# Optimization experiments

Measured on AMD Instinct MI355X. Metric: run time of the kernel, lower is better.

## Reference

```python
import jax, jax.numpy as jnp
import numpy as np

N, E, B, NUM_NODES = 80000, 1280000, 8, 10000
D_IN, H, EMB, ATT, OUT = 64, 64, 64, 64, 1


def setup_inputs() -> dict:
    key = jax.random.key(0)
    ks = jax.random.split(key, 12)
    x = jax.random.normal(ks[0], (N, D_IN), dtype=jnp.float32)
    edge_index = jax.random.randint(ks[1], (2, E), 0, N, dtype=jnp.int64)
    edge_weight = jax.random.uniform(ks[2], (E,), dtype=jnp.float32)
    batch = jnp.repeat(jnp.arange(B, dtype=jnp.int64), NUM_NODES)
    app_embedding = jax.random.normal(ks[3], (B, 1, EMB), dtype=jnp.float32)
    def lin(k, fi, fo):
        bound = 1.0 / np.sqrt(fi)
        k1, k2 = jax.random.split(k)
        W = jax.random.uniform(k1, (fi, fo), minval=-bound, maxval=bound, dtype=jnp.float32)
        b = jax.random.uniform(k2, (fo,), minval=-bound, maxval=bound, dtype=jnp.float32)
        return W, b
    W1, b1 = lin(ks[4], D_IN, H)
    W2, b2 = lin(ks[5], H, H)
    Wa, ba = lin(ks[6], H + EMB, ATT)
    Ws, bs = lin(ks[7], ATT, 1)
    Wo, bo = lin(ks[8], H, OUT)
    return dict(x=x, edge_index=edge_index, edge_weight=edge_weight, batch=batch,
                app_embedding=app_embedding, W1=W1, b1=b1, W2=W2, b2=b2,
                Wa=Wa, ba=ba, Ws=Ws, bs=bs, Wo=Wo, bo=bo)


def gcn_conv(x, row, col, ew, W, b):
    # PyG GCNConv: add self-loops (weight 1), symmetric normalization
    n = x.shape[0]
    xw = x @ W                                            # [N, H]
    deg = jax.ops.segment_sum(ew, col, num_segments=n) + 1.0  # self-loop adds 1
    dis = jax.lax.rsqrt(deg)                              # deg >= 1
    norm = dis[row] * ew * dis[col]                       # [E]
    agg = jax.ops.segment_sum(norm[:, None] * xw[row], col, num_segments=n)
    return agg + (dis * dis)[:, None] * xw + b            # self-loop term + bias


def reference(x, edge_index, edge_weight, batch, app_embedding,
              W1, b1, W2, b2, Wa, ba, Ws, bs, Wo, bo):
    row, col = edge_index[0], edge_index[1]
    h = jax.nn.relu(gcn_conv(x, row, col, edge_weight, W1, b1))
    h = jax.nn.relu(gcn_conv(h, row, col, edge_weight, W2, b2))
    emb = app_embedding[:, 0, :][batch]                   # [N, EMB]
    combined = jnp.concatenate([h, emb], axis=-1)         # [N, H+EMB]
    att_hidden = jax.nn.leaky_relu(combined @ Wa + ba, negative_slope=0.2)
    scores = att_hidden @ Ws + bs                         # [N, 1]
    weights = jax.nn.softmax(scores, axis=0)              # softmax over all nodes
    node_out = (weights * h) @ Wo + bo                    # [N, OUT=1]
    flat = node_out.reshape(-1)                           # [N] since OUT=1
    sums = jax.ops.segment_sum(flat, batch, num_segments=B)
    counts = jax.ops.segment_sum(jnp.ones_like(flat), batch, num_segments=B)
    return sums / counts                                  # global_mean_pool -> [B]
```

## Files before the change

### kernel.cpp

```cpp
#include <hip/hip_runtime.h>
#include <hip/hip_fp16.h>
#include <math.h>


#define DEG_SCALE 16777216.0f
#define DEG_INV   (1.0f / 16777216.0f)
#define M48       0xFFFFFFFFFFFFULL
#define MAXDEG    64

typedef __attribute__((ext_vector_type(8))) _Float16 h8;
typedef __attribute__((ext_vector_type(4))) float f32x4;


__global__ __launch_bounds__(256) void front_kernel(
    const float* __restrict__ x, const float* __restrict__ W1,
    __half* __restrict__ Y, int N,
    const int* __restrict__ ei, const float* __restrict__ ew,
    unsigned long long* __restrict__ packed, unsigned int* __restrict__ epack2,
    int E, int nG) {
  int bid = (int)blockIdx.x;
  bool isGemm = (bid % 5 == 0) && (bid / 5 < nG);
  if (!isGemm) {
    int gBefore = (bid + 4) / 5; if (gBefore > nG) gBefore = nG;
    int di = bid - gBefore;
    int e = di * 256 + threadIdx.x;
    if (e >= E) return;
    int row = ei[e];
    int col = ei[E + e];
    float w = ew[e];
    unsigned long long q = (unsigned long long)(w * DEG_SCALE + 0.5f);
    unsigned long long old = atomicAdd(&packed[col], (1ULL << 48) | q);
    unsigned rank = (unsigned)(old >> 48);
    unsigned q15 = (unsigned)(w * 32768.0f + 0.5f);
    if (q15 > 32767u) q15 = 32767u;
    if (rank < MAXDEG)
      epack2[(size_t)col * MAXDEG + rank] = ((unsigned)row << 15) | q15;
    return;
  }
  int gb = bid / 5;
  __shared__ float wlds[64][65];
  int t = threadIdx.x;
  for (int i = t; i < 4096; i += 256) wlds[i >> 6][i & 63] = W1[i];
  __syncthreads();
  int lane = t & 63, wave = t >> 6;
  int sub = lane & 15, grp = lane >> 4;
  int r0 = gb * 64 + wave * 16;
  h8 bf[2][4];
#pragma unroll
  for (int kk = 0; kk < 2; ++kk)
#pragma unroll
    for (int f = 0; f < 4; ++f)
#pragma unroll
      for (int i = 0; i < 8; ++i)
        bf[kk][f][i] = (_Float16)wlds[kk * 32 + grp * 8 + i][f * 16 + sub];
  int arow = r0 + sub; if (arow >= N) arow = N - 1;
  const float4* xr = (const float4*)(x + (size_t)arow * 64 + grp * 8);
  float4 u0 = xr[0], u1 = xr[1];
  const float4* xr2 = (const float4*)(x + (size_t)arow * 64 + 32 + grp * 8);
  float4 v0 = xr2[0], v1 = xr2[1];
  h8 a0, a1;
  a0[0]=(_Float16)u0.x; a0[1]=(_Float16)u0.y; a0[2]=(_Float16)u0.z; a0[3]=(_Float16)u0.w;
  a0[4]=(_Float16)u1.x; a0[5]=(_Float16)u1.y; a0[6]=(_Float16)u1.z; a0[7]=(_Float16)u1.w;
  a1[0]=(_Float16)v0.x; a1[1]=(_Float16)v0.y; a1[2]=(_Float16)v0.z; a1[3]=(_Float16)v0.w;
  a1[4]=(_Float16)v1.x; a1[5]=(_Float16)v1.y; a1[6]=(_Float16)v1.z; a1[7]=(_Float16)v1.w;
  f32x4 zero = {0.f, 0.f, 0.f, 0.f};
  f32x4 acc[4] = {zero, zero, zero, zero};
#pragma unroll
  for (int f = 0; f < 4; ++f) {
    acc[f] = __builtin_amdgcn_mfma_f32_16x16x32_f16(a0, bf[0][f], acc[f], 0, 0, 0);
    acc[f] = __builtin_amdgcn_mfma_f32_16x16x32_f16(a1, bf[1][f], acc[f], 0, 0, 0);
  }
  _Float16* Yp = (_Float16*)Y;
#pragma unroll
  for (int f = 0; f < 4; ++f)
#pragma unroll
    for (int j = 0; j < 4; ++j) {
      int orow = r0 + grp * 4 + j;
      if (orow < N) Yp[(size_t)orow * 64 + f * 16 + sub] = (_Float16)acc[f][j];
    }
}

__global__ __launch_bounds__(256) void mid_kernel(
    const unsigned long long* __restrict__ packed, __half* __restrict__ xw,
    float* __restrict__ dis, int N,
    const float* __restrict__ emb, const float* __restrict__ Wa,
    const float* __restrict__ ba, float* __restrict__ pre, int B, int gS) {
  if ((int)blockIdx.x >= gS) {
    int t = ((int)blockIdx.x - gS) * 256 + threadIdx.x;
    if (t >= B * 64) return;
    int b = t >> 6, j = t & 63;
    float s = ba[j];
    for (int k = 0; k < 64; ++k)
      s = fmaf(emb[b * 64 + k], Wa[(64 + k) * 64 + j], s);
    pre[t] = s;
    return;
  }
  int idx = blockIdx.x * 256 + threadIdx.x;
  if (idx >= N * 8) return;
  int row = idx >> 3;
  int off = idx & 7;
  unsigned long long p = packed[row];
  float d = rsqrtf((float)(long long)(p & M48) * DEG_INV + 1.0f);
  if (off == 0) dis[row] = d;
  h8* ptr = (h8*)(xw + (size_t)row * 64) + off;
  h8 v = *ptr;
  h8 o;
#pragma unroll
  for (int i = 0; i < 8; ++i) o[i] = (_Float16)((float)v[i] * d);
  *ptr = o;
}

__global__ __launch_bounds__(256) void agg_fused_kernel(
    const __half* __restrict__ xw, const unsigned int* __restrict__ epack2,
    const unsigned long long* __restrict__ packed,
    const float* __restrict__ bias, __half* __restrict__ h, int N) {
  int wid = (blockIdx.x * 256 + threadIdx.x) >> 6;
  int lane = threadIdx.x & 63;
  if (wid >= N) return;
  int q = lane >> 3, sub = lane & 7;
  unsigned long long p = packed[wid];
  int cnt = (int)(p >> 48);
  if (cnt > MAXDEG) cnt = MAXDEG;
  float dis_c = rsqrtf((float)(long long)(p & M48) * DEG_INV + 1.0f);
  int start = wid * MAXDEG;
  int end = start + cnt;
  float acc[8];
#pragma unroll
  for (int i = 0; i < 8; ++i) acc[i] = 0.f;
  int t = start + q;
  for (; t + 8 < end; t += 16) {
    unsigned w0 = epack2[t];
    unsigned w1 = epack2[t + 8];
    h8 v0 = *(const h8*)(xw + ((size_t)(w0 >> 15)) * 64 + sub * 8);
    h8 v1 = *(const h8*)(xw + ((size_t)(w1 >> 15)) * 64 + sub * 8);
    float c0 = (float)(w0 & 0x7FFFu) * (1.0f / 32768.0f);
    float c1 = (float)(w1 & 0x7FFFu) * (1.0f / 32768.0f);
#pragma unroll
    for (int i = 0; i < 8; ++i) acc[i] = fmaf(c0, (float)v0[i], acc[i]);
#pragma unroll
    for (int i = 0; i < 8; ++i) acc[i] = fmaf(c1, (float)v1[i], acc[i]);
  }
  if (t < end) {
    unsigned w0 = epack2[t];
    h8 v0 = *(const h8*)(xw + ((size_t)(w0 >> 15)) * 64 + sub * 8);
    float c0 = (float)(w0 & 0x7FFFu) * (1.0f / 32768.0f);
#pragma unroll
    for (int i = 0; i < 8; ++i) acc[i] = fmaf(c0, (float)v0[i], acc[i]);
  }
#pragma unroll
  for (int i = 0; i < 8; ++i) {
    acc[i] += __shfl_xor(acc[i], 8, 64);
    acc[i] += __shfl_xor(acc[i], 16, 64);
    acc[i] += __shfl_xor(acc[i], 32, 64);
  }
  if (q == 0) {
    h8 self = *(const h8*)(xw + (size_t)wid * 64 + sub * 8);
    h8 o;
#pragma unroll
    for (int i = 0; i < 8; ++i)
      o[i] = (_Float16)fmaxf(dis_c * (acc[i] + (float)self[i]) + bias[sub * 8 + i], 0.f);
    *(h8*)(h + (size_t)wid * 64 + sub * 8) = o;
  }
}

__global__ __launch_bounds__(256) void gemm_mfma_f16_scaled(
    const __half* __restrict__ X, const float* __restrict__ W,
    const float* __restrict__ dis, __half* __restrict__ Y, int N) {
  __shared__ float wlds[64][65];
  int t = threadIdx.x;
  for (int i = t; i < 4096; i += 256) wlds[i >> 6][i & 63] = W[i];
  __syncthreads();
  int lane = t & 63, wave = t >> 6;
  int sub = lane & 15, grp = lane >> 4;
  int r0 = (int)blockIdx.x * 64 + wave * 16;
  h8 bf[2][4];
#pragma unroll
  for (int kk = 0; kk < 2; ++kk)
#pragma unroll
    for (int f = 0; f < 4; ++f)
#pragma unroll
      for (int i = 0; i < 8; ++i)
        bf[kk][f][i] = (_Float16)wlds[kk * 32 + grp * 8 + i][f * 16 + sub];
  int arow = r0 + sub; if (arow >= N) arow = N - 1;
  const _Float16* Xp = (const _Float16*)X;
  h8 a0 = *(const h8*)(Xp + (size_t)arow * 64 + grp * 8);
  h8 a1 = *(const h8*)(Xp + (size_t)arow * 64 + 32 + grp * 8);
  f32x4 zero = {0.f, 0.f, 0.f, 0.f};
  f32x4 acc[4] = {zero, zero, zero, zero};
#pragma unroll
  for (int f = 0; f < 4; ++f) {
    acc[f] = __builtin_amdgcn_mfma_f32_16x16x32_f16(a0, bf[0][f], acc[f], 0, 0, 0);
    acc[f] = __builtin_amdgcn_mfma_f32_16x16x32_f16(a1, bf[1][f], acc[f], 0, 0, 0);
  }
  _Float16* Yp = (_Float16*)Y;
#pragma unroll
  for (int j = 0; j < 4; ++j) {
    int orow = r0 + grp * 4 + j;
    if (orow < N) {
      float d = dis[orow];
#pragma unroll
      for (int f = 0; f < 4; ++f)
        Yp[(size_t)orow * 64 + f * 16 + sub] = (_Float16)(acc[f][j] * d);
    }
  }
}

__global__ __launch_bounds__(256) void att_mfma_kernel(
    const __half* __restrict__ h2, const int* __restrict__ bat,
    const float* __restrict__ Wa, const float* __restrict__ Ws,
    const float* __restrict__ bs, const float* __restrict__ pre,
    const float* __restrict__ Wo,
    float* __restrict__ bmax, float* __restrict__ bsum,
    float* __restrict__ pd0, float* __restrict__ pd1, int N) {
  __shared__ float wlds[64][65];
  __shared__ float pr[8][64];
  __shared__ float wov[64];
  __shared__ float redm[4], reds[4], redp0[4], redp1[4];
  __shared__ int sb0sh;
  int t = threadIdx.x;
  for (int i = t; i < 4096; i += 256) wlds[i >> 6][i & 63] = Wa[i];
  for (int i = t; i < 512; i += 256) pr[i >> 6][i & 63] = pre[i];
  if (t < 64) wov[t] = Wo[t];
  if (t == 0) sb0sh = bat[blockIdx.x * 64];
  __syncthreads();
  int lane = t & 63, wave = t >> 6;
  int sub = lane & 15, grp = lane >> 4;
  int r0 = (int)blockIdx.x * 64 + wave * 16;
  h8 bf[2][4];
#pragma unroll
  for (int kk = 0; kk < 2; ++kk)
#pragma unroll
    for (int f = 0; f < 4; ++f)
#pragma unroll
      for (int i = 0; i < 8; ++i)
        bf[kk][f][i] = (_Float16)wlds[kk * 32 + grp * 8 + i][f * 16 + sub];
  float wsf[4];
#pragma unroll
  for (int f = 0; f < 4; ++f) wsf[f] = Ws[f * 16 + sub];
  float bs0 = bs[0];
  int arow = r0 + sub; if (arow >= N) arow = N - 1;
  const _Float16* Xp = (const _Float16*)h2;
  h8 a0 = *(const h8*)(Xp + (size_t)arow * 64 + grp * 8);
  h8 a1 = *(const h8*)(Xp + (size_t)arow * 64 + 32 + grp * 8);
  float dp = 0.f;
#pragma unroll
  for (int i = 0; i < 8; ++i) {
    dp = fmaf((float)a0[i], wov[grp * 8 + i], dp);
    dp = fmaf((float)a1[i], wov[32 + grp * 8 + i], dp);
  }
  dp += __shfl_xor(dp, 16, 64);
  dp += __shfl_xor(dp, 32, 64);
  f32x4 zero = {0.f, 0.f, 0.f, 0.f};
  f32x4 acc[4] = {zero, zero, zero, zero};
#pragma unroll
  for (int f = 0; f < 4; ++f) {
    acc[f] = __builtin_amdgcn_mfma_f32_16x16x32_f16(a0, bf[0][f], acc[f], 0, 0, 0);
    acc[f] = __builtin_amdgcn_mfma_f32_16x16x32_f16(a1, bf[1][f], acc[f], 0, 0, 0);
  }
  int sb0 = sb0sh;
  float sloc[4];
  int bl[4];
  float mloc = -3.4e38f;
#pragma unroll
  for (int j = 0; j < 4; ++j) {
    int row = r0 + grp * 4 + j;
    int rc = (row < N) ? row : N - 1;
    int b = bat[rc];
    bl[j] = b;
    float s = 0.f;
#pragma unroll
    for (int f = 0; f < 4; ++f) {
      float v = acc[f][j] + pr[b][f * 16 + sub];
      v = (v > 0.f) ? v : 0.2f * v;
      s = fmaf(v, wsf[f], s);
    }
    s += __shfl_xor(s, 1, 64); s += __shfl_xor(s, 2, 64);
    s += __shfl_xor(s, 4, 64); s += __shfl_xor(s, 8, 64);
    s += bs0;
    sloc[j] = (row < N) ? s : -3.4e38f;
    mloc = fmaxf(mloc, sloc[j]);
  }
  for (int off = 32; off; off >>= 1) mloc = fmaxf(mloc, __shfl_xor(mloc, off, 64));
  if (lane == 0) redm[wave] = mloc;
  __syncthreads();
  float bm = fmaxf(fmaxf(redm[0], redm[1]), fmaxf(redm[2], redm[3]));
  float dj[4];
#pragma unroll
  for (int j = 0; j < 4; ++j) dj[j] = __shfl(dp, grp * 4 + j, 64);
  float es = 0.f, p0 = 0.f, p1 = 0.f;
  if (sub == 0) {
#pragma unroll
    for (int j = 0; j < 4; ++j) {
      if (sloc[j] > -3.0e38f) {
        float e = expf(sloc[j] - bm);
        es += e;
        float v = e * dj[j];
        if (bl[j] == sb0) p0 += v; else p1 += v;
      }
    }
  }
  for (int off = 32; off; off >>= 1) {
    es += __shfl_xor(es, off, 64);
    p0 += __shfl_xor(p0, off, 64);
    p1 += __shfl_xor(p1, off, 64);
  }
  if (lane == 0) { reds[wave] = es; redp0[wave] = p0; redp1[wave] = p1; }
  __syncthreads();
  if (t == 0) {
    bmax[blockIdx.x] = bm;
    bsum[blockIdx.x] = reds[0] + reds[1] + reds[2] + reds[3];
    pd0[blockIdx.x] = redp0[0] + redp0[1] + redp0[2] + redp0[3];
    pd1[blockIdx.x] = redp1[0] + redp1[1] + redp1[2] + redp1[3];
  }
}

__global__ __launch_bounds__(256) void tail_kernel(
    const float* __restrict__ bmax, const float* __restrict__ bsum,
    const float* __restrict__ pd0, const float* __restrict__ pd1,
    int nb, int npb, const float* __restrict__ bo, float* __restrict__ out, int B) {
  __shared__ float lds[4];
  __shared__ float Msh, Zsh;
  __shared__ float accs[9];
  int t = threadIdx.x;
  if (t < 9) accs[t] = 0.f;
  float m = -3.4e38f;
  for (int k = t; k < nb; k += 256) m = fmaxf(m, bmax[k]);
  for (int off = 32; off; off >>= 1) m = fmaxf(m, __shfl_xor(m, off, 64));
  if ((t & 63) == 0) lds[t >> 6] = m;
  __syncthreads();
  if (t == 0) Msh = fmaxf(fmaxf(lds[0], lds[1]), fmaxf(lds[2], lds[3]));
  __syncthreads();
  float M = Msh;
  float z = 0.f;
  for (int k = t; k < nb; k += 256) {
    float e = expf(bmax[k] - M);
    z += bsum[k] * e;
    int b0 = (k * 64) / npb;
    float v0 = pd0[k] * e;
    float v1 = pd1[k] * e;
    if (v0 != 0.f) atomicAdd(&accs[b0], v0);
    if (v1 != 0.f) atomicAdd(&accs[b0 + 1], v1);
  }
  for (int off = 32; off; off >>= 1) z += __shfl_xor(z, off, 64);
  if ((t & 63) == 0) lds[t >> 6] = z;
  __syncthreads();
  if (t == 0) Zsh = lds[0] + lds[1] + lds[2] + lds[3];
  __syncthreads();
  if (t < B) out[t] = accs[t] / Zsh / (float)npb + bo[0];
}

extern "C" void kernel_launch(void* const* d_in, const int* in_sizes, int n_in,
                              void* d_out, int out_size, void* d_ws, size_t ws_size,
                              hipStream_t stream) {
  const float* x   = (const float*)d_in[0];
  const int*   ei  = (const int*)d_in[1];
  const float* ew  = (const float*)d_in[2];
  const int*   bat = (const int*)d_in[3];
  const float* emb = (const float*)d_in[4];
  const float* W1  = (const float*)d_in[5];
  const float* b1  = (const float*)d_in[6];
  const float* W2  = (const float*)d_in[7];
  const float* b2  = (const float*)d_in[8];
  const float* Wa  = (const float*)d_in[9];
  const float* ba  = (const float*)d_in[10];
  const float* Ws  = (const float*)d_in[11];
  const float* bs  = (const float*)d_in[12];
  const float* Wo  = (const float*)d_in[13];
  const float* bo  = (const float*)d_in[14];
  float* out = (float*)d_out;

  const int N = in_sizes[0] / 64;
  const int E = in_sizes[2];
  const int B = in_sizes[4] / 64;

  float* ws = (float*)d_ws;
  size_t o = 0;
  unsigned long long* packed = (unsigned long long*)(ws + o); o += 2 * (size_t)N;
  unsigned int* epack2 = (unsigned int*)(ws + o); o += (size_t)N * MAXDEG;
  __half* bufA   = (__half*)(ws + o); o += (size_t)N * 32;
  __half* bufB   = (__half*)(ws + o); o += (size_t)N * 32;
  float* dis     = ws + o; o += N;
  float* pre     = ws + o; o += 512;
  float* bmaxa   = ws + o; o += 2048;
  float* bsuma   = ws + o; o += 2048;
  float* pd0a    = ws + o; o += 2048;
  float* pd1a    = ws + o; o += 2048;

  hipMemsetAsync(packed, 0, (size_t)(2 * N) * sizeof(float), stream);

  int gE = (E + 255) / 256;
  int gW = (N * 64 + 255) / 256;
  int gM = (N + 63) / 64;
  int gS = (N * 8 + 255) / 256;
  int gP = (B * 64 + 255) / 256;

  front_kernel<<<gM + gE, 256, 0, stream>>>(x, W1, bufA, N, ei, ew, packed, epack2, E, gM);

  mid_kernel<<<gS + gP, 256, 0, stream>>>(packed, bufA, dis, N, emb, Wa, ba, pre, B, gS);

  agg_fused_kernel<<<gW, 256, 0, stream>>>(bufA, epack2, packed, b1, bufB, N);
  gemm_mfma_f16_scaled<<<gM, 256, 0, stream>>>(bufB, W2, dis, bufA, N);
  agg_fused_kernel<<<gW, 256, 0, stream>>>(bufA, epack2, packed, b2, bufB, N);

  att_mfma_kernel<<<gM, 256, 0, stream>>>(bufB, bat, Wa, Ws, bs, pre, Wo,
                                          bmaxa, bsuma, pd0a, pd1a, N);
  tail_kernel<<<1, 256, 0, stream>>>(bmaxa, bsuma, pd0a, pd1a, gM, N / B, bo, out, B);
}
```

Baseline: 199.4 us.

## Fuse GCN aggregation with following dense layers and drop pre-scaling pass

After: 371.6 us. 86.4% more time.

```diff
diff --git a/kernel.cpp b/kernel.cpp
--- a/kernel.cpp
+++ b/kernel.cpp
@@ -7,10 +7,10 @@
 #define DEG_INV   (1.0f / 16777216.0f)
 #define M48       0xFFFFFFFFFFFFULL
 #define MAXDEG    64
+#define NPB       32
 
 typedef __attribute__((ext_vector_type(8))) _Float16 h8;
 typedef __attribute__((ext_vector_type(4))) float f32x4;
-
 
 __global__ __launch_bounds__(256) void front_kernel(
     const float* __restrict__ x, const float* __restrict__ W1,
@@ -80,13 +80,12 @@
     }
 }
 
-__global__ __launch_bounds__(256) void mid_kernel(
-    const unsigned long long* __restrict__ packed, __half* __restrict__ xw,
-    float* __restrict__ dis, int N,
+__global__ __launch_bounds__(256) void mid2_kernel(
+    const unsigned long long* __restrict__ packed, float* __restrict__ dis, int N,
     const float* __restrict__ emb, const float* __restrict__ Wa,
-    const float* __restrict__ ba, float* __restrict__ pre, int B, int gS) {
-  if ((int)blockIdx.x >= gS) {
-    int t = ((int)blockIdx.x - gS) * 256 + threadIdx.x;
+    const float* __restrict__ ba, float* __restrict__ pre, int B, int gD) {
+  if ((int)blockIdx.x >= gD) {
+    int t = ((int)blockIdx.x - gD) * 256 + threadIdx.x;
     if (t >= B * 64) return;
     int b = t >> 6, j = t & 63;
     float s = ba[j];
@@ -95,55 +94,41 @@
     pre[t] = s;
     return;
   }
-  int idx = blockIdx.x * 256 + threadIdx.x;
-  if (idx >= N * 8) return;
-  int row = idx >> 3;
-  int off = idx & 7;
-  unsigned long long p = packed[row];
-  float d = rsqrtf((float)(long long)(p & M48) * DEG_INV + 1.0f);
-  if (off == 0) dis[row] = d;
-  h8* ptr = (h8*)(xw + (size_t)row * 64) + off;
-  h8 v = *ptr;
-  h8 o;
-#pragma unroll
-  for (int i = 0; i < 8; ++i) o[i] = (_Float16)((float)v[i] * d);
-  *ptr = o;
-}
-
-__global__ __launch_bounds__(256) void agg_fused_kernel(
+  int i = blockIdx.x * 256 + threadIdx.x;
+  if (i >= N) return;
+  unsigned long long p = packed[i];
+  dis[i] = rsqrtf((float)(long long)(p & M48) * DEG_INV + 1.0f);
+}
+
+__device__ __forceinline__ void gather_node(
     const __half* __restrict__ xw, const unsigned int* __restrict__ epack2,
-    const unsigned long long* __restrict__ packed,
-    const float* __restrict__ bias, __half* __restrict__ h, int N) {
-  int wid = (blockIdx.x * 256 + threadIdx.x) >> 6;
-  int lane = threadIdx.x & 63;
-  if (wid >= N) return;
-  int q = lane >> 3, sub = lane & 7;
-  unsigned long long p = packed[wid];
-  int cnt = (int)(p >> 48);
-  if (cnt > MAXDEG) cnt = MAXDEG;
-  float dis_c = rsqrtf((float)(long long)(p & M48) * DEG_INV + 1.0f);
+    const float* __restrict__ dis, int wid, int cnt, int q, int sub,
+    float acc[8]) {
+#pragma unroll
+  for (int i = 0; i < 8; ++i) acc[i] = 0.f;
   int start = wid * MAXDEG;
   int end = start + cnt;
-  float acc[8];
-#pragma unroll
-  for (int i = 0; i < 8; ++i) acc[i] = 0.f;
-  int t = start + q;
-  for (; t + 8 < end; t += 16) {
-    unsigned w0 = epack2[t];
-    unsigned w1 = epack2[t + 8];
-    h8 v0 = *(const h8*)(xw + ((size_t)(w0 >> 15)) * 64 + sub * 8);
-    h8 v1 = *(const h8*)(xw + ((size_t)(w1 >> 15)) * 64 + sub * 8);
-    float c0 = (float)(w0 & 0x7FFFu) * (1.0f / 32768.0f);
-    float c1 = (float)(w1 & 0x7FFFu) * (1.0f / 32768.0f);
+  int e = start + q;
+  for (; e + 8 < end; e += 16) {
+    unsigned w0 = epack2[e];
+    unsigned w1 = epack2[e + 8];
+    int r0 = (int)(w0 >> 15), r1 = (int)(w1 >> 15);
+    float d0 = dis[r0], d1 = dis[r1];
+    h8 v0 = *(const h8*)(xw + (size_t)r0 * 64 + sub * 8);
+    h8 v1 = *(const h8*)(xw + (size_t)r1 * 64 + sub * 8);
+    float c0 = (float)(w0 & 0x7FFFu) * (1.0f / 32768.0f) * d0;
+    float c1 = (float)(w1 & 0x7FFFu) * (1.0f / 32768.0f) * d1;
 #pragma unroll
     for (int i = 0; i < 8; ++i) acc[i] = fmaf(c0, (float)v0[i], acc[i]);
 #pragma unroll
     for (int i = 0; i < 8; ++i) acc[i] = fmaf(c1, (float)v1[i], acc[i]);
   }
-  if (t < end) {
-    unsigned w0 = epack2[t];
-    h8 v0 = *(const h8*)(xw + ((size_t)(w0 >> 15)) * 64 + sub * 8);
-    float c0 = (float)(w0 & 0x7FFFu) * (1.0f / 32768.0f);
+  if (e < end) {
+    unsigned w0 = epack2[e];
+    int r0 = (int)(w0 >> 15);
+    float d0 = dis[r0];
+    h8 v0 = *(const h8*)(xw + (size_t)r0 * 64 + sub * 8);
+    float c0 = (float)(w0 & 0x7FFFu) * (1.0f / 32768.0f) * d0;
 #pragma unroll
     for (int i = 0; i < 8; ++i) acc[i] = fmaf(c0, (float)v0[i], acc[i]);
   }
@@ -153,164 +138,127 @@
     acc[i] += __shfl_xor(acc[i], 16, 64);
     acc[i] += __shfl_xor(acc[i], 32, 64);
   }
-  if (q == 0) {
+}
+
+__global__ __launch_bounds__(256) void conv_gemm_kernel(
+    const __half* __restrict__ xw, const unsigned int* __restrict__ epack2,
+    const unsigned long long* __restrict__ packed, const float* __restrict__ dis,
+    const float* __restrict__ b1, const float* __restrict__ W2,
+    __half* __restrict__ xw2, int N) {
+  __shared__ float w2[64][65];
+  int t = threadIdx.x;
+  for (int i = t; i < 4096; i += 256) w2[i >> 6][i & 63] = W2[i];
+  __syncthreads();
+  int lane = t & 63, wave = t >> 6;
+  int q = lane >> 3, sub = lane & 7;
+  float bias[8];
+#pragma unroll
+  for (int i = 0; i < 8; ++i) bias[i] = b1[sub * 8 + i];
+  int base = (int)blockIdx.x * NPB;
+  for (int n = wave; n < NPB; n += 4) {
+    int wid = base + n;
+    if (wid >= N) break;
+    unsigned long long p = packed[wid];
+    int cnt = (int)(p >> 48); if (cnt > MAXDEG) cnt = MAXDEG;
+    float dis_c = dis[wid];
+    float acc[8];
+    gather_node(xw, epack2, dis, wid, cnt, q, sub, acc);
     h8 self = *(const h8*)(xw + (size_t)wid * 64 + sub * 8);
-    h8 o;
+    float dc2 = dis_c * dis_c;
+    float h1v[8];
 #pragma unroll
     for (int i = 0; i < 8; ++i)
-      o[i] = (_Float16)fmaxf(dis_c * (acc[i] + (float)self[i]) + bias[sub * 8 + i], 0.f);
-    *(h8*)(h + (size_t)wid * 64 + sub * 8) = o;
-  }
-}
-
-__global__ __launch_bounds__(256) void gemm_mfma_f16_scaled(
-    const __half* __restrict__ X, const float* __restrict__ W,
-    const float* __restrict__ dis, __half* __restrict__ Y, int N) {
-  __shared__ float wlds[64][65];
-  int t = threadIdx.x;
-  for (int i = t; i < 4096; i += 256) wlds[i >> 6][i & 63] = W[i];
-  __syncthreads();
-  int lane = t & 63, wave = t >> 6;
-  int sub = lane & 15, grp = lane >> 4;
-  int r0 = (int)blockIdx.x * 64 + wave * 16;
-  h8 bf[2][4];
-#pragma unroll
-  for (int kk = 0; kk < 2; ++kk)
-#pragma unroll
-    for (int f = 0; f < 4; ++f)
+      h1v[i] = fmaxf(fmaf(dis_c, acc[i], fmaf(dc2, (float)self[i], bias[i])), 0.f);
+    float y = 0.f;
+#pragma unroll
+    for (int s = 0; s < 8; ++s)
 #pragma unroll
       for (int i = 0; i < 8; ++i)
-        bf[kk][f][i] = (_Float16)wlds[kk * 32 + grp * 8 + i][f * 16 + sub];
-  int arow = r0 + sub; if (arow >= N) arow = N - 1;
-  const _Float16* Xp = (const _Float16*)X;
-  h8 a0 = *(const h8*)(Xp + (size_t)arow * 64 + grp * 8);
-  h8 a1 = *(const h8*)(Xp + (size_t)arow * 64 + 32 + grp * 8);
-  f32x4 zero = {0.f, 0.f, 0.f, 0.f};
-  f32x4 acc[4] = {zero, zero, zero, zero};
-#pragma unroll
-  for (int f = 0; f < 4; ++f) {
-    acc[f] = __builtin_amdgcn_mfma_f32_16x16x32_f16(a0, bf[0][f], acc[f], 0, 0, 0);
-    acc[f] = __builtin_amdgcn_mfma_f32_16x16x32_f16(a1, bf[1][f], acc[f], 0, 0, 0);
-  }
-  _Float16* Yp = (_Float16*)Y;
-#pragma unroll
-  for (int j = 0; j < 4; ++j) {
-    int orow = r0 + grp * 4 + j;
-    if (orow < N) {
-      float d = dis[orow];
-#pragma unroll
-      for (int f = 0; f < 4; ++f)
-        Yp[(size_t)orow * 64 + f * 16 + sub] = (_Float16)(acc[f][j] * d);
-    }
-  }
-}
-
-__global__ __launch_bounds__(256) void att_mfma_kernel(
-    const __half* __restrict__ h2, const int* __restrict__ bat,
+        y = fmaf(__shfl(h1v[i], s, 64), w2[s * 8 + i][lane], y);
+    ((_Float16*)xw2)[(size_t)wid * 64 + lane] = (_Float16)y;
+  }
+}
+
+__global__ __launch_bounds__(256) void conv_att_kernel(
+    const __half* __restrict__ xw2, const unsigned int* __restrict__ epack2,
+    const unsigned long long* __restrict__ packed, const float* __restrict__ dis,
+    const float* __restrict__ b2, const int* __restrict__ bat,
     const float* __restrict__ Wa, const float* __restrict__ Ws,
     const float* __restrict__ bs, const float* __restrict__ pre,
     const float* __restrict__ Wo,
     float* __restrict__ bmax, float* __restrict__ bsum,
     float* __restrict__ pd0, float* __restrict__ pd1, int N) {
-  __shared__ float wlds[64][65];
+  __shared__ float wa[64][65];
   __shared__ float pr[8][64];
-  __shared__ float wov[64];
-  __shared__ float redm[4], reds[4], redp0[4], redp1[4];
+  __shared__ float wsv[64], wov[64];
+  __shared__ float cm[4], cz[4], cp0[4], cp1[4];
   __shared__ int sb0sh;
   int t = threadIdx.x;
-  for (int i = t; i < 4096; i += 256) wlds[i >> 6][i & 63] = Wa[i];
+  for (int i = t; i < 4096; i += 256) wa[i >> 6][i & 63] = Wa[i];
   for (int i = t; i < 512; i += 256) pr[i >> 6][i & 63] = pre[i];
-  if (t < 64) wov[t] = Wo[t];
-  if (t == 0) sb0sh = bat[blockIdx.x * 64];
+  if (t < 64) { wsv[t] = Ws[t]; wov[t] = Wo[t]; }
+  if (t == 0) sb0sh = bat[(size_t)blockIdx.x * NPB];
   __syncthreads();
   int lane = t & 63, wave = t >> 6;
-  int sub = lane & 15, grp = lane >> 4;
-  int r0 = (int)blockIdx.x * 64 + wave * 16;
-  h8 bf[2][4];
-#pragma unroll
-  for (int kk = 0; kk < 2; ++kk)
-#pragma unroll
-    for (int f = 0; f < 4; ++f)
-#pragma unroll
-      for (int i = 0; i < 8; ++i)
-        bf[kk][f][i] = (_Float16)wlds[kk * 32 + grp * 8 + i][f * 16 + sub];
-  float wsf[4];
-#pragma unroll
-  for (int f = 0; f < 4; ++f) wsf[f] = Ws[f * 16 + sub];
+  int q = lane >> 3, sub = lane & 7;
+  float bias[8];
+#pragma unroll
+  for (int i = 0; i < 8; ++i) bias[i] = b2[sub * 8 + i];
   float bs0 = bs[0];
-  int arow = r0 + sub; if (arow >= N) arow = N - 1;
-  const _Float16* Xp = (const _Float16*)h2;
-  h8 a0 = *(const h8*)(Xp + (size_t)arow * 64 + grp * 8);
-  h8 a1 = *(const h8*)(Xp + (size_t)arow * 64 + 32 + grp * 8);
-  float dp = 0.f;
-#pragma unroll
-  for (int i = 0; i < 8; ++i) {
-    dp = fmaf((float)a0[i], wov[grp * 8 + i], dp);
-    dp = fmaf((float)a1[i], wov[32 + grp * 8 + i], dp);
-  }
-  dp += __shfl_xor(dp, 16, 64);
-  dp += __shfl_xor(dp, 32, 64);
-  f32x4 zero = {0.f, 0.f, 0.f, 0.f};
-  f32x4 acc[4] = {zero, zero, zero, zero};
-#pragma unroll
-  for (int f = 0; f < 4; ++f) {
-    acc[f] = __builtin_amdgcn_mfma_f32_16x16x32_f16(a0, bf[0][f], acc[f], 0, 0, 0);
-    acc[f] = __builtin_amdgcn_mfma_f32_16x16x32_f16(a1, bf[1][f], acc[f], 0, 0, 0);
-  }
   int sb0 = sb0sh;
-  float sloc[4];
-  int bl[4];
-  float mloc = -3.4e38f;
-#pragma unroll
-  for (int j = 0; j < 4; ++j) {
-    int row = r0 + grp * 4 + j;
-    int rc = (row < N) ? row : N - 1;
-    int b = bat[rc];
-    bl[j] = b;
-    float s = 0.f;
-#pragma unroll
-    for (int f = 0; f < 4; ++f) {
-      float v = acc[f][j] + pr[b][f * 16 + sub];
-      v = (v > 0.f) ? v : 0.2f * v;
-      s = fmaf(v, wsf[f], s);
+  float m = -3.4e38f, z = 0.f, p0 = 0.f, p1 = 0.f;
+  int base = (int)blockIdx.x * NPB;
+  for (int n = wave; n < NPB; n += 4) {
+    int wid = base + n;
+    if (wid >= N) break;
+    unsigned long long p = packed[wid];
+    int cnt = (int)(p >> 48); if (cnt > MAXDEG) cnt = MAXDEG;
+    float dis_c = dis[wid];
+    float acc[8];
+    gather_node(xw2, epack2, dis, wid, cnt, q, sub, acc);
+    h8 self = *(const h8*)(xw2 + (size_t)wid * 64 + sub * 8);
+    float dc2 = dis_c * dis_c;
+    float h2v[8];
+#pragma unroll
+    for (int i = 0; i < 8; ++i)
+      h2v[i] = fmaxf(fmaf(dis_c, acc[i], fmaf(dc2, (float)self[i], bias[i])), 0.f);
+    int b = bat[wid];
+    float y = pr[b][lane];
+    float dp = 0.f;
+#pragma unroll
+    for (int s = 0; s < 8; ++s)
+#pragma unroll
+      for (int i = 0; i < 8; ++i) {
+        float hv = __shfl(h2v[i], s, 64);
+        y = fmaf(hv, wa[s * 8 + i][lane], y);
+        dp = fmaf(hv, wov[s * 8 + i], dp);
+      }
+    float a = ((y > 0.f) ? y : 0.2f * y) * wsv[lane];
+    a += __shfl_xor(a, 1, 64);  a += __shfl_xor(a, 2, 64);
+    a += __shfl_xor(a, 4, 64);  a += __shfl_xor(a, 8, 64);
+    a += __shfl_xor(a, 16, 64); a += __shfl_xor(a, 32, 64);
+    float s_r = a + bs0;
+    if (s_r > m) {
+      float r = expf(m - s_r);
+      z *= r; p0 *= r; p1 *= r; m = s_r;
     }
-    s += __shfl_xor(s, 1, 64); s += __shfl_xor(s, 2, 64);
-    s += __shfl_xor(s, 4, 64); s += __shfl_xor(s, 8, 64);
-    s += bs0;
-    sloc[j] = (row < N) ? s : -3.4e38f;
-    mloc = fmaxf(mloc, sloc[j]);
-  }
-  for (int off = 32; off; off >>= 1) mloc = fmaxf(mloc, __shfl_xor(mloc, off, 64));
-  if (lane == 0) redm[wave] = mloc;
-  __syncthreads();
-  float bm = fmaxf(fmaxf(redm[0], redm[1]), fmaxf(redm[2], redm[3]));
-  float dj[4];
-#pragma unroll
-  for (int j = 0; j < 4; ++j) dj[j] = __shfl(dp, grp * 4 + j, 64);
-  float es = 0.f, p0 = 0.f, p1 = 0.f;
-  if (sub == 0) {
-#pragma unroll
-    for (int j = 0; j < 4; ++j) {
-      if (sloc[j] > -3.0e38f) {
-        float e = expf(sloc[j] - bm);
-        es += e;
-        float v = e * dj[j];
-        if (bl[j] == sb0) p0 += v; else p1 += v;
-      }
+    float e = expf(s_r - m);
+    z += e;
+    float v = e * dp;
+    if (b == sb0) p0 += v; else p1 += v;
+  }
+  if (lane == 0) { cm[wave] = m; cz[wave] = z; cp0[wave] = p0; cp1[wave] = p1; }
+  __syncthreads();
+  if (t == 0) {
+    float M = fmaxf(fmaxf(cm[0], cm[1]), fmaxf(cm[2], cm[3]));
+    float Z = 0.f, P0 = 0.f, P1 = 0.f;
+#pragma unroll
+    for (int w = 0; w < 4; ++w) {
+      float e = expf(cm[w] - M);
+      Z += cz[w] * e; P0 += cp0[w] * e; P1 += cp1[w] * e;
     }
-  }
-  for (int off = 32; off; off >>= 1) {
-    es += __shfl_xor(es, off, 64);
-    p0 += __shfl_xor(p0, off, 64);
-    p1 += __shfl_xor(p1, off, 64);
-  }
-  if (lane == 0) { reds[wave] = es; redp0[wave] = p0; redp1[wave] = p1; }
-  __syncthreads();
-  if (t == 0) {
-    bmax[blockIdx.x] = bm;
-    bsum[blockIdx.x] = reds[0] + reds[1] + reds[2] + reds[3];
-    pd0[blockIdx.x] = redp0[0] + redp0[1] + redp0[2] + redp0[3];
-    pd1[blockIdx.x] = redp1[0] + redp1[1] + redp1[2] + redp1[3];
+    bmax[blockIdx.x] = M; bsum[blockIdx.x] = Z;
+    pd0[blockIdx.x] = P0; pd1[blockIdx.x] = P1;
   }
 }
 
@@ -335,7 +283,7 @@
   for (int k = t; k < nb; k += 256) {
     float e = expf(bmax[k] - M);
     z += bsum[k] * e;
-    int b0 = (k * 64) / npb;
+    int b0 = (k * NPB) / npb;
     float v0 = pd0[k] * e;
     float v1 = pd1[k] * e;
     if (v0 != 0.f) atomicAdd(&accs[b0], v0);
@@ -378,31 +326,31 @@
   unsigned long long* packed = (unsigned long long*)(ws + o); o += 2 * (size_t)N;
   unsigned int* epack2 = (unsigned int*)(ws + o); o += (size_t)N * MAXDEG;
   __half* bufA   = (__half*)(ws + o); o += (size_t)N * 32;
-  __half* bufB   = (__half*)(ws + o); o += (size_t)N * 32;
+  __half* bufX2  = (__half*)(ws + o); o += (size_t)N * 32;
   float* dis     = ws + o; o += N;
   float* pre     = ws + o; o += 512;
-  float* bmaxa   = ws + o; o += 2048;
-  float* bsuma   = ws + o; o += 2048;
-  float* pd0a    = ws + o; o += 2048;
-  float* pd1a    = ws + o; o += 2048;
+  float* bmaxa   = ws + o; o += 4096;
+  float* bsuma   = ws + o; o += 4096;
+  float* pd0a    = ws + o; o += 4096;
+  float* pd1a    = ws + o; o += 4096;
 
   hipMemsetAsync(packed, 0, (size_t)(2 * N) * sizeof(float), stream);
 
   int gE = (E + 255) / 256;
-  int gW = (N * 64 + 255) / 256;
   int gM = (N + 63) / 64;
-  int gS = (N * 8 + 255) / 256;
+  int gD = (N + 255) / 256;
   int gP = (B * 64 + 255) / 256;
+  int nc = (N + NPB - 1) / NPB;
 
   front_kernel<<<gM + gE, 256, 0, stream>>>(x, W1, bufA, N, ei, ew, packed, epack2, E, gM);
 
-  mid_kernel<<<gS + gP, 256, 0, stream>>>(packed, bufA, dis, N, emb, Wa, ba, pre, B, gS);
-
-  agg_fused_kernel<<<gW, 256, 0, stream>>>(bufA, epack2, packed, b1, bufB, N);
-  gemm_mfma_f16_scaled<<<gM, 256, 0, stream>>>(bufB, W2, dis, bufA, N);
-  agg_fused_kernel<<<gW, 256, 0, stream>>>(bufA, epack2, packed, b2, bufB, N);
-
-  att_mfma_kernel<<<gM, 256, 0, stream>>>(bufB, bat, Wa, Ws, bs, pre, Wo,
+  mid2_kernel<<<gD + gP, 256, 0, stream>>>(packed, dis, N, emb, Wa, ba, pre, B, gD);
+
+  conv_gemm_kernel<<<nc, 256, 0, stream>>>(bufA, epack2, packed, dis, b1, W2, bufX2, N);
+
+  conv_att_kernel<<<nc, 256, 0, stream>>>(bufX2, epack2, packed, dis, b2, bat,
+                                          Wa, Ws, bs, pre, Wo,
                                           bmaxa, bsuma, pd0a, pd1a, N);
-  tail_kernel<<<1, 256, 0, stream>>>(bmaxa, bsuma, pd0a, pd1a, gM, N / B, bo, out, B);
-}
+
+  tail_kernel<<<1, 256, 0, stream>>>(bmaxa, bsuma, pd0a, pd1a, nc, N / B, bo, out, B);
+}
```
